# Kernel optimization log

Measured on AMD Instinct MI355X. Metric: run time of the kernel, lower is better.

The kernel has to match this reference:

```python
import jax, jax.numpy as jnp
import numpy as np

B, T, D, H = 128, 1024, 128, 512

def setup_inputs() -> dict:
    key = jax.random.key(0)
    ks = jax.random.split(key, 7)
    s = 1.0 / np.sqrt(H)
    return {
        "x":    jax.random.normal(ks[0], (B, T, D), dtype=jnp.float32),
        "W_ih": jax.random.uniform(ks[1], (4 * H, D), jnp.float32, -s, s),
        "W_hh": jax.random.uniform(ks[2], (4 * H, H), jnp.float32, -s, s),
        "b_ih": jax.random.uniform(ks[3], (4 * H,), jnp.float32, -s, s),
        "b_hh": jax.random.uniform(ks[4], (4 * H,), jnp.float32, -s, s),
        "W_fc": jax.random.uniform(ks[5], (1, H), jnp.float32, -s, s),
        "b_fc": jax.random.uniform(ks[6], (1,), jnp.float32, -s, s),
    }

def _lstm_last_hidden(x, W_ih, W_hh, b_ih, b_hh):
    # Precompute input-side gate projections for all timesteps: [T, B, 4H]
    xg = jnp.einsum('btd,gd->tbg', x, W_ih) + (b_ih + b_hh)
    Bq = x.shape[0]
    Hq = W_hh.shape[1]
    h0 = jnp.zeros((Bq, Hq), x.dtype)
    c0 = jnp.zeros((Bq, Hq), x.dtype)

    def step(carry, g_in):
        h, c = carry
        g = g_in + h @ W_hh.T                      # [B, 4H]
        i, f, gc, o = jnp.split(g, 4, axis=-1)     # PyTorch gate order i,f,g,o
        i = jax.nn.sigmoid(i)
        f = jax.nn.sigmoid(f)
        gc = jnp.tanh(gc)
        o = jax.nn.sigmoid(o)
        c = f * c + i * gc
        h = o * jnp.tanh(c)
        return (h, c), None

    (h_last, _), _ = jax.lax.scan(step, (h0, c0), xg)
    return h_last

def reference(x, W_ih, W_hh, b_ih, b_hh, W_fc, b_fc):
    h = _lstm_last_hidden(x, W_ih, W_hh, b_ih, b_hh)   # out[:, -1, :]
    return jax.nn.sigmoid(h @ W_fc.T + b_fc)           # [B, 1]
```

## Files before the change

### kernel.cpp

```cpp
#include <hip/hip_runtime.h>
#include <hip/hip_bf16.h>

#define Bsz 128
#define Tsz 1024
#define Dsz 128
#define Hsz 512
#define NBLK 256
#define NKC 20

typedef __attribute__((ext_vector_type(8))) short short8;
typedef __attribute__((ext_vector_type(4))) float f4;
typedef unsigned long long u64;

__device__ __forceinline__ short bf16_rne(float f) {
  unsigned u = __builtin_bit_cast(unsigned, f);
  u += 0x7fffu + ((u >> 16) & 1u);
  return (short)(u >> 16);
}
__device__ __forceinline__ float sigmoid_(float v) { return 1.f / (1.f + __expf(-v)); }
__device__ __forceinline__ float tanh_fast(float v) {
  return 1.f - 2.f / (1.f + __expf(2.f * v));
}

__global__ __launch_bounds__(256, 1) void lstm_persist(
    const float* __restrict__ x, const float* __restrict__ W_ih,
    const float* __restrict__ W_hh, const float* __restrict__ b_ih,
    const float* __restrict__ b_hh, const float* __restrict__ W_fc,
    const float* __restrict__ b_fc, float* __restrict__ out,
    int* flags, unsigned short* hb0, unsigned short* hb1)
{
  const int bx = blockIdx.x;
  const int bt = bx & 7, ks = bx >> 3;
  const int b0 = bt << 4, k0 = ks << 4;
  const int tx = threadIdx.x;
  const int wave = tx >> 6, lane = tx & 63;
  const int m = lane & 15, quad = lane >> 4;
  const int k_l = tx & 15, b_l = tx >> 4;

  __shared__ short8 A_lds[NKC][64];
  __shared__ float fc_red[16][16];

  int* gflags = flags + bt * 32;

  const int mycol = k0 + wave * 4 + (m & 3);
  short8 wfrag[NKC];
  {
    const int j = (m >> 2) * Hsz + mycol;
    #pragma unroll
    for (int kc = 0; kc < NKC; ++kc) {
      const int kk = kc * 32 + quad * 8;
      const float* src = (kk < Dsz) ? (W_ih + (size_t)j * Dsz + kk)
                                    : (W_hh + (size_t)j * Hsz + (kk - Dsz));
      const f4* sv = (const f4*)src;
      f4 v0 = sv[0], v1 = sv[1];
      short8 w;
      w[0] = bf16_rne(v0[0]); w[1] = bf16_rne(v0[1]);
      w[2] = bf16_rne(v0[2]); w[3] = bf16_rne(v0[3]);
      w[4] = bf16_rne(v1[0]); w[5] = bf16_rne(v1[1]);
      w[6] = bf16_rne(v1[2]); w[7] = bf16_rne(v1[3]);
      wfrag[kc] = w;
    }
  }
  float bias[4];
  #pragma unroll
  for (int g = 0; g < 4; ++g)
    bias[g] = b_ih[g * Hsz + mycol] + b_hh[g * Hsz + mycol];
  float c_reg = 0.f;

  for (int t = 0; t < Tsz; ++t) {
    unsigned short* hnext = (t & 1) ? hb1 : hb0;
    const unsigned short* hprev = (t & 1) ? hb0 : hb1;

    const f4* xv = (const f4*)(x + (size_t)(b0 + m) * (Tsz * Dsz)
                               + (size_t)t * Dsz + wave * 32 + quad * 8);
    f4 v0 = xv[0], v1 = xv[1];

    if (t > 0) {
      for (;;) {
        int f = __hip_atomic_load(gflags + (lane & 31),
                                  __ATOMIC_RELAXED, __HIP_MEMORY_SCOPE_AGENT);
        if (__all(f >= t)) break;
        __builtin_amdgcn_s_sleep(1);
      }
      #pragma unroll
      for (int q = 0; q < 4; ++q) {
        const int kc = 4 + wave * 4 + q;
        const int kh = (kc - 4) * 32 + quad * 8;
        const u64* p = (const u64*)(hprev + (size_t)(b0 + m) * Hsz + kh);
        u64 lo = __hip_atomic_load(p,     __ATOMIC_RELAXED, __HIP_MEMORY_SCOPE_AGENT);
        u64 hi = __hip_atomic_load(p + 1, __ATOMIC_RELAXED, __HIP_MEMORY_SCOPE_AGENT);
        u64* dst = (u64*)&A_lds[kc][lane];
        dst[0] = lo; dst[1] = hi;
      }
    } else {
      short8 z = {0, 0, 0, 0, 0, 0, 0, 0};
      #pragma unroll
      for (int q = 0; q < 4; ++q) A_lds[4 + wave * 4 + q][lane] = z;
    }

    {
      short8 a;
      a[0] = bf16_rne(v0[0]); a[1] = bf16_rne(v0[1]);
      a[2] = bf16_rne(v0[2]); a[3] = bf16_rne(v0[3]);
      a[4] = bf16_rne(v1[0]); a[5] = bf16_rne(v1[1]);
      a[6] = bf16_rne(v1[2]); a[7] = bf16_rne(v1[3]);
      A_lds[wave][lane] = a;
    }
    __syncthreads();

    f4 a0 = {0.f, 0.f, 0.f, 0.f}, a1 = {0.f, 0.f, 0.f, 0.f};
    f4 a2 = {0.f, 0.f, 0.f, 0.f}, a3 = {0.f, 0.f, 0.f, 0.f};
    #pragma unroll
    for (int kc = 0; kc < NKC; kc += 4) {
      a0 = __builtin_amdgcn_mfma_f32_16x16x32_bf16(A_lds[kc][lane],     wfrag[kc],     a0, 0, 0, 0);
      a1 = __builtin_amdgcn_mfma_f32_16x16x32_bf16(A_lds[kc + 1][lane], wfrag[kc + 1], a1, 0, 0, 0);
      a2 = __builtin_amdgcn_mfma_f32_16x16x32_bf16(A_lds[kc + 2][lane], wfrag[kc + 2], a2, 0, 0, 0);
      a3 = __builtin_amdgcn_mfma_f32_16x16x32_bf16(A_lds[kc + 3][lane], wfrag[kc + 3], a3, 0, 0, 0);
    }
    f4 acc = (a0 + a1) + (a2 + a3);

    {
      const int g0b = (m >> 2) & 1, g1b = (m >> 3) & 1;
      float s1[4], v1[4];
      #pragma unroll
      for (int r = 0; r < 4; ++r) s1[r] = __shfl_xor(acc[r ^ 1], 4);
      #pragma unroll
      for (int r = 0; r < 4; ++r) v1[r] = ((r & 1) == g0b) ? acc[r] : s1[r];
      float s2[4], v2[4];
      #pragma unroll
      for (int r = 0; r < 4; ++r) s2[r] = __shfl_xor(v1[r ^ 2], 8);
      #pragma unroll
      for (int r = 0; r < 4; ++r) v2[r] = (((r >> 1) & 1) == g1b) ? v1[r] : s2[r];
      float pi = v2[0] + bias[0];
      float pf = v2[1] + bias[1];
      float pg = v2[2] + bias[2];
      float po = v2[3] + bias[3];
      float iv = sigmoid_(pi), fv = sigmoid_(pf), ov = sigmoid_(po);
      float gv = tanh_fast(pg);
      c_reg = fv * c_reg + iv * gv;
      float hv = ov * tanh_fast(c_reg);
      unsigned hbits = (unsigned)(unsigned short)bf16_rne(hv);
      unsigned lo = hbits | (__shfl_xor(hbits, 1) << 16);
      u64 both = ((u64)__shfl_xor(lo, 2) << 32) | (u64)lo;
      if ((m & 3) == 0) {
        const int brow = b0 + quad * 4 + (m >> 2);
        u64* p = (u64*)(hnext + (size_t)brow * Hsz + k0 + wave * 4);
        __hip_atomic_store(p, both, __ATOMIC_RELAXED, __HIP_MEMORY_SCOPE_AGENT);
      }
    }
    __syncthreads();
    if (tx == 0)
      __hip_atomic_store(gflags + ks, t + 1, __ATOMIC_RELAXED, __HIP_MEMORY_SCOPE_AGENT);
  }

  if (ks == 0) {
    for (;;) {
      int f = __hip_atomic_load(gflags + (lane & 31),
                                __ATOMIC_RELAXED, __HIP_MEMORY_SCOPE_AGENT);
      if (__all(f >= Tsz)) break;
      __builtin_amdgcn_s_sleep(1);
    }
    const unsigned short* hl = hb1;
    const u64* p = (const u64*)(hl + (size_t)(b0 + b_l) * Hsz + k_l * 32);
    float partial = 0.f;
    #pragma unroll
    for (int q = 0; q < 8; ++q) {
      u64 v = __hip_atomic_load(p + q, __ATOMIC_RELAXED, __HIP_MEMORY_SCOPE_AGENT);
      #pragma unroll
      for (int e = 0; e < 4; ++e) {
        unsigned hv16 = (unsigned)((v >> (16 * e)) & 0xffffu);
        partial += __builtin_bit_cast(float, hv16 << 16) * W_fc[k_l * 32 + q * 4 + e];
      }
    }
    fc_red[b_l][k_l] = partial;
    __syncthreads();
    if (k_l == 0) {
      float s = b_fc[0];
      #pragma unroll
      for (int e = 0; e < 16; ++e) s += fc_red[b_l][e];
      out[b0 + b_l] = sigmoid_(s);
    }
  }
}

extern "C" void kernel_launch(void* const* d_in, const int* in_sizes, int n_in,
                              void* d_out, int out_size, void* d_ws, size_t ws_size,
                              hipStream_t stream) {
  const float* x    = (const float*)d_in[0];
  const float* W_ih = (const float*)d_in[1];
  const float* W_hh = (const float*)d_in[2];
  const float* b_ih = (const float*)d_in[3];
  const float* b_hh = (const float*)d_in[4];
  const float* W_fc = (const float*)d_in[5];
  const float* b_fc = (const float*)d_in[6];
  float* out = (float*)d_out;
  char* ws = (char*)d_ws;
  int* flags = (int*)ws;
  unsigned short* hb0 = (unsigned short*)(ws + 4096);
  unsigned short* hb1 = (unsigned short*)(ws + 4096 + (size_t)Bsz * Hsz * 2);
  hipMemsetAsync(ws, 0, 4096, stream);
  lstm_persist<<<NBLK, 256, 0, stream>>>(x, W_ih, W_hh, b_ih, b_hh, W_fc, b_fc,
                                         out, flags, hb0, hb1);
}
```

Measured before the change: 3.167 ms.

## Halve persistent block count by giving each wave two hidden-column groups

Each block now computes 32 hidden columns instead of 16, so the grid shrinks from 256 to 128 persistent blocks and each batch tile waits on 16 flags instead of 32. Each wave keeps two sets of weight fragments in registers and issues twice the MFMAs per step, reusing each LDS A fragment for both sets. The aim is to cut the cross-block flag polling and synchronisation cost per timestep, at the price of doubling per-block MFMA and gate work on the serial path and higher register pressure.

```diff
diff --git a/kernel.cpp b/kernel.cpp
--- a/kernel.cpp
+++ b/kernel.cpp
@@ -5,7 +5,7 @@
 #define Tsz 1024
 #define Dsz 128
 #define Hsz 512
-#define NBLK 256
+#define NBLK 128
 #define NKC 20
 
 typedef __attribute__((ext_vector_type(8))) short short8;
@@ -31,7 +31,7 @@
 {
   const int bx = blockIdx.x;
   const int bt = bx & 7, ks = bx >> 3;
-  const int b0 = bt << 4, k0 = ks << 4;
+  const int b0 = bt << 4, k0 = ks << 5;
   const int tx = threadIdx.x;
   const int wave = tx >> 6, lane = tx & 63;
   const int m = lane & 15, quad = lane >> 4;
@@ -40,32 +40,46 @@
   __shared__ short8 A_lds[NKC][64];
   __shared__ float fc_red[16][16];
 
-  int* gflags = flags + bt * 32;
-
-  const int mycol = k0 + wave * 4 + (m & 3);
-  short8 wfrag[NKC];
+  int* gflags = flags + bt * 16;
+
+  const int colA = k0 + wave * 8 + (m & 3);
+  const int colB = colA + 4;
+  short8 wfragA[NKC], wfragB[NKC];
   {
-    const int j = (m >> 2) * Hsz + mycol;
+    const int jA = (m >> 2) * Hsz + colA;
+    const int jB = (m >> 2) * Hsz + colB;
     #pragma unroll
     for (int kc = 0; kc < NKC; ++kc) {
       const int kk = kc * 32 + quad * 8;
-      const float* src = (kk < Dsz) ? (W_ih + (size_t)j * Dsz + kk)
-                                    : (W_hh + (size_t)j * Hsz + (kk - Dsz));
-      const f4* sv = (const f4*)src;
-      f4 v0 = sv[0], v1 = sv[1];
-      short8 w;
-      w[0] = bf16_rne(v0[0]); w[1] = bf16_rne(v0[1]);
-      w[2] = bf16_rne(v0[2]); w[3] = bf16_rne(v0[3]);
-      w[4] = bf16_rne(v1[0]); w[5] = bf16_rne(v1[1]);
-      w[6] = bf16_rne(v1[2]); w[7] = bf16_rne(v1[3]);
-      wfrag[kc] = w;
-    }
-  }
-  float bias[4];
+      const float* srcA = (kk < Dsz) ? (W_ih + (size_t)jA * Dsz + kk)
+                                     : (W_hh + (size_t)jA * Hsz + (kk - Dsz));
+      const float* srcB = (kk < Dsz) ? (W_ih + (size_t)jB * Dsz + kk)
+                                     : (W_hh + (size_t)jB * Hsz + (kk - Dsz));
+      const f4* svA = (const f4*)srcA;
+      f4 va0 = svA[0], va1 = svA[1];
+      short8 wa;
+      wa[0] = bf16_rne(va0[0]); wa[1] = bf16_rne(va0[1]);
+      wa[2] = bf16_rne(va0[2]); wa[3] = bf16_rne(va0[3]);
+      wa[4] = bf16_rne(va1[0]); wa[5] = bf16_rne(va1[1]);
+      wa[6] = bf16_rne(va1[2]); wa[7] = bf16_rne(va1[3]);
+      wfragA[kc] = wa;
+      const f4* svB = (const f4*)srcB;
+      f4 vb0 = svB[0], vb1 = svB[1];
+      short8 wb;
+      wb[0] = bf16_rne(vb0[0]); wb[1] = bf16_rne(vb0[1]);
+      wb[2] = bf16_rne(vb0[2]); wb[3] = bf16_rne(vb0[3]);
+      wb[4] = bf16_rne(vb1[0]); wb[5] = bf16_rne(vb1[1]);
+      wb[6] = bf16_rne(vb1[2]); wb[7] = bf16_rne(vb1[3]);
+      wfragB[kc] = wb;
+    }
+  }
+  float biasA[4], biasB[4];
   #pragma unroll
-  for (int g = 0; g < 4; ++g)
-    bias[g] = b_ih[g * Hsz + mycol] + b_hh[g * Hsz + mycol];
-  float c_reg = 0.f;
+  for (int g = 0; g < 4; ++g) {
+    biasA[g] = b_ih[g * Hsz + colA] + b_hh[g * Hsz + colA];
+    biasB[g] = b_ih[g * Hsz + colB] + b_hh[g * Hsz + colB];
+  }
+  float c_regA = 0.f, c_regB = 0.f;
 
   for (int t = 0; t < Tsz; ++t) {
     unsigned short* hnext = (t & 1) ? hb1 : hb0;
@@ -77,7 +91,7 @@
 
     if (t > 0) {
       for (;;) {
-        int f = __hip_atomic_load(gflags + (lane & 31),
+        int f = __hip_atomic_load(gflags + (lane & 15),
                                   __ATOMIC_RELAXED, __HIP_MEMORY_SCOPE_AGENT);
         if (__all(f >= t)) break;
         __builtin_amdgcn_s_sleep(1);
@@ -108,44 +122,72 @@
     }
     __syncthreads();
 
-    f4 a0 = {0.f, 0.f, 0.f, 0.f}, a1 = {0.f, 0.f, 0.f, 0.f};
-    f4 a2 = {0.f, 0.f, 0.f, 0.f}, a3 = {0.f, 0.f, 0.f, 0.f};
+    f4 a0 = {0.f,0.f,0.f,0.f}, a1 = {0.f,0.f,0.f,0.f};
+    f4 a2 = {0.f,0.f,0.f,0.f}, a3 = {0.f,0.f,0.f,0.f};
+    f4 c0 = {0.f,0.f,0.f,0.f}, c1 = {0.f,0.f,0.f,0.f};
+    f4 c2 = {0.f,0.f,0.f,0.f}, c3 = {0.f,0.f,0.f,0.f};
     #pragma unroll
     for (int kc = 0; kc < NKC; kc += 4) {
-      a0 = __builtin_amdgcn_mfma_f32_16x16x32_bf16(A_lds[kc][lane],     wfrag[kc],     a0, 0, 0, 0);
-      a1 = __builtin_amdgcn_mfma_f32_16x16x32_bf16(A_lds[kc + 1][lane], wfrag[kc + 1], a1, 0, 0, 0);
-      a2 = __builtin_amdgcn_mfma_f32_16x16x32_bf16(A_lds[kc + 2][lane], wfrag[kc + 2], a2, 0, 0, 0);
-      a3 = __builtin_amdgcn_mfma_f32_16x16x32_bf16(A_lds[kc + 3][lane], wfrag[kc + 3], a3, 0, 0, 0);
-    }
-    f4 acc = (a0 + a1) + (a2 + a3);
+      short8 f0 = A_lds[kc][lane],     f1 = A_lds[kc + 1][lane];
+      short8 f2 = A_lds[kc + 2][lane], f3 = A_lds[kc + 3][lane];
+      a0 = __builtin_amdgcn_mfma_f32_16x16x32_bf16(f0, wfragA[kc],     a0, 0, 0, 0);
+      c0 = __builtin_amdgcn_mfma_f32_16x16x32_bf16(f0, wfragB[kc],     c0, 0, 0, 0);
+      a1 = __builtin_amdgcn_mfma_f32_16x16x32_bf16(f1, wfragA[kc + 1], a1, 0, 0, 0);
+      c1 = __builtin_amdgcn_mfma_f32_16x16x32_bf16(f1, wfragB[kc + 1], c1, 0, 0, 0);
+      a2 = __builtin_amdgcn_mfma_f32_16x16x32_bf16(f2, wfragA[kc + 2], a2, 0, 0, 0);
+      c2 = __builtin_amdgcn_mfma_f32_16x16x32_bf16(f2, wfragB[kc + 2], c2, 0, 0, 0);
+      a3 = __builtin_amdgcn_mfma_f32_16x16x32_bf16(f3, wfragA[kc + 3], a3, 0, 0, 0);
+      c3 = __builtin_amdgcn_mfma_f32_16x16x32_bf16(f3, wfragB[kc + 3], c3, 0, 0, 0);
+    }
+    f4 accA = (a0 + a1) + (a2 + a3);
+    f4 accB = (c0 + c1) + (c2 + c3);
 
     {
       const int g0b = (m >> 2) & 1, g1b = (m >> 3) & 1;
-      float s1[4], v1[4];
-      #pragma unroll
-      for (int r = 0; r < 4; ++r) s1[r] = __shfl_xor(acc[r ^ 1], 4);
-      #pragma unroll
-      for (int r = 0; r < 4; ++r) v1[r] = ((r & 1) == g0b) ? acc[r] : s1[r];
-      float s2[4], v2[4];
-      #pragma unroll
-      for (int r = 0; r < 4; ++r) s2[r] = __shfl_xor(v1[r ^ 2], 8);
-      #pragma unroll
-      for (int r = 0; r < 4; ++r) v2[r] = (((r >> 1) & 1) == g1b) ? v1[r] : s2[r];
-      float pi = v2[0] + bias[0];
-      float pf = v2[1] + bias[1];
-      float pg = v2[2] + bias[2];
-      float po = v2[3] + bias[3];
-      float iv = sigmoid_(pi), fv = sigmoid_(pf), ov = sigmoid_(po);
-      float gv = tanh_fast(pg);
-      c_reg = fv * c_reg + iv * gv;
-      float hv = ov * tanh_fast(c_reg);
-      unsigned hbits = (unsigned)(unsigned short)bf16_rne(hv);
-      unsigned lo = hbits | (__shfl_xor(hbits, 1) << 16);
-      u64 both = ((u64)__shfl_xor(lo, 2) << 32) | (u64)lo;
+      float vA[4], vB[4];
+      {
+        float s1[4], w1[4];
+        #pragma unroll
+        for (int r = 0; r < 4; ++r) s1[r] = __shfl_xor(accA[r ^ 1], 4);
+        #pragma unroll
+        for (int r = 0; r < 4; ++r) w1[r] = ((r & 1) == g0b) ? accA[r] : s1[r];
+        float s2[4];
+        #pragma unroll
+        for (int r = 0; r < 4; ++r) s2[r] = __shfl_xor(w1[r ^ 2], 8);
+        #pragma unroll
+        for (int r = 0; r < 4; ++r) vA[r] = (((r >> 1) & 1) == g1b) ? w1[r] : s2[r];
+      }
+      {
+        float s1[4], w1[4];
+        #pragma unroll
+        for (int r = 0; r < 4; ++r) s1[r] = __shfl_xor(accB[r ^ 1], 4);
+        #pragma unroll
+        for (int r = 0; r < 4; ++r) w1[r] = ((r & 1) == g0b) ? accB[r] : s1[r];
+        float s2[4];
+        #pragma unroll
+        for (int r = 0; r < 4; ++r) s2[r] = __shfl_xor(w1[r ^ 2], 8);
+        #pragma unroll
+        for (int r = 0; r < 4; ++r) vB[r] = (((r >> 1) & 1) == g1b) ? w1[r] : s2[r];
+      }
+      float iA = sigmoid_(vA[0] + biasA[0]), fA = sigmoid_(vA[1] + biasA[1]);
+      float gA = tanh_fast(vA[2] + biasA[2]), oA = sigmoid_(vA[3] + biasA[3]);
+      c_regA = fA * c_regA + iA * gA;
+      float hA = oA * tanh_fast(c_regA);
+      float iB = sigmoid_(vB[0] + biasB[0]), fB = sigmoid_(vB[1] + biasB[1]);
+      float gB = tanh_fast(vB[2] + biasB[2]), oB = sigmoid_(vB[3] + biasB[3]);
+      c_regB = fB * c_regB + iB * gB;
+      float hB = oB * tanh_fast(c_regB);
+      unsigned hbA = (unsigned)(unsigned short)bf16_rne(hA);
+      unsigned loA = hbA | (__shfl_xor(hbA, 1) << 16);
+      u64 bothA = ((u64)__shfl_xor(loA, 2) << 32) | (u64)loA;
+      unsigned hbB = (unsigned)(unsigned short)bf16_rne(hB);
+      unsigned loB = hbB | (__shfl_xor(hbB, 1) << 16);
+      u64 bothB = ((u64)__shfl_xor(loB, 2) << 32) | (u64)loB;
       if ((m & 3) == 0) {
         const int brow = b0 + quad * 4 + (m >> 2);
-        u64* p = (u64*)(hnext + (size_t)brow * Hsz + k0 + wave * 4);
-        __hip_atomic_store(p, both, __ATOMIC_RELAXED, __HIP_MEMORY_SCOPE_AGENT);
+        u64* p = (u64*)(hnext + (size_t)brow * Hsz + k0 + wave * 8);
+        __hip_atomic_store(p,     bothA, __ATOMIC_RELAXED, __HIP_MEMORY_SCOPE_AGENT);
+        __hip_atomic_store(p + 1, bothB, __ATOMIC_RELAXED, __HIP_MEMORY_SCOPE_AGENT);
       }
     }
     __syncthreads();
@@ -155,7 +197,7 @@
 
   if (ks == 0) {
     for (;;) {
-      int f = __hip_atomic_load(gflags + (lane & 31),
+      int f = __hip_atomic_load(gflags + (lane & 15),
                                 __ATOMIC_RELAXED, __HIP_MEMORY_SCOPE_AGENT);
       if (__all(f >= Tsz)) break;
       __builtin_amdgcn_s_sleep(1);
```

Result: slower. 3.575 ms (+12.9%).
